# Optimization experiments

Hardware: AMD Instinct MI355X
Metric: run time of the kernel (lower is better)

## Reference

```python
import jax, jax.numpy as jnp
import numpy as np

B, T, SD, AD, H, K, HID = 256, 128, 8, 2, 3, 4, 256


def setup_inputs() -> dict:
    key = jax.random.key(0)
    ks = jax.random.split(key, 12)
    inp = {
        "state": jax.random.normal(ks[0], (B, T, SD), dtype=jnp.float32),
        "action": jax.random.normal(ks[1], (B, T, AD), dtype=jnp.float32),
        # Linear(4, 4*H, bias=False): weight (4*H, 4)
        "Wk": jax.random.normal(ks[2], (4 * H, K), dtype=jnp.float32) * 0.1,
        "Wq": jax.random.normal(ks[3], (4 * H, SD + AD), dtype=jnp.float32) * 0.1,
        "Wv": jax.random.normal(ks[4], (4 * H, K), dtype=jnp.float32) * 0.1,
        # MLP: in_dim = 4*H + SD + AD -> HID -> HID -> 1
        "W1": jax.random.normal(ks[5], (HID, 4 * H + SD + AD), dtype=jnp.float32) * 0.05,
        "b1": jnp.zeros((HID,), dtype=jnp.float32),
        "W2": jax.random.normal(ks[6], (HID, HID), dtype=jnp.float32) * 0.05,
        "b2": jnp.zeros((HID,), dtype=jnp.float32),
        "Wout": jax.random.uniform(ks[7], (1, HID), minval=-0.003, maxval=0.003, dtype=jnp.float32),
        "bout": jax.random.uniform(ks[8], (1,), minval=-0.003, maxval=0.003, dtype=jnp.float32),
    }
    return inp


def reference(state, action, Wk, Wq, Wv, W1, b1, W2, b2, Wout, bout):
    q_state = jnp.concatenate([state, action], axis=-1)  # (b, t, sd+ad)
    s = state[:, :, :4]                                   # (b, t, 4)
    b, t, k = s.shape
    h = Wk.shape[0] // k
    # rel_full[b, i, j] = s[b, j] - s[b, i]  (matches torch view/transpose)
    rel_full = s[:, None, :, :] - s[:, :, None, :]        # (b, t, t, 4)
    # drop diagonal (self-pairs): idx[i] = all j != i, in order
    j = jnp.arange(t - 1)
    idx = j[None, :] + (j[None, :] >= jnp.arange(t)[:, None])  # (t, t-1)
    rel = jnp.take_along_axis(rel_full, idx[None, :, :, None], axis=2)  # (b, t, t-1, 4)
    # QKV projections (tiny head dim k=4)
    q = (q_state @ Wq.T).reshape(b, t, h, k)              # (b, t, h, 4)
    keys = (rel @ Wk.T).reshape(b, t, t - 1, h, k)        # (b, t, t-1, h, 4)
    vals = (rel @ Wv.T).reshape(b, t, t - 1, h, k)
    scores = jnp.einsum('bthk,btjhk->bthj', q, keys) / jnp.sqrt(jnp.float32(k))
    w = jax.nn.softmax(scores, axis=-1)                   # over the t-1 neighbors
    x = jnp.einsum('bthj,btjhk->bthk', w, vals).reshape(b, t, h * k)
    x = jnp.concatenate([x, q_state], axis=-1)            # (b, t, h*4 + sd+ad)
    x = jax.nn.relu(x @ W1.T + b1)
    x = jax.nn.relu(x @ W2.T + b2)
    return x @ Wout.T + bout                              # (b, t, 1)
```

## Files before the change

kernel.cpp:

```cpp
#include <hip/hip_runtime.h>
#include <math.h>

#define Bp 256
#define Tp 128
#define SDp 8
#define ADp 2
#define Hp 3
#define Kp 4
#define HIDp 256
#define QDp (SDp + ADp)
#define X1Dp (Hp * Kp + QDp)
#define QKLD 17
#define LOG2E 1.4426950408889634f

typedef short bf16x8 __attribute__((ext_vector_type(8)));
typedef float f32x4  __attribute__((ext_vector_type(4)));

__device__ __forceinline__ unsigned short f2bf(float f) {
    unsigned u = __float_as_uint(f);
    unsigned r = (u + 0x7FFFu + ((u >> 16) & 1u)) >> 16;
    return (unsigned short)r;
}

__device__ __forceinline__ unsigned h1_byte(int row, int colbytes) {
    return (((unsigned)row << 9) + (unsigned)colbytes) ^ ((unsigned)(row & 7) << 4);
}
__device__ __forceinline__ unsigned x1_byte(int row, int colbytes) {
    return ((unsigned)row << 6) + ((unsigned)colbytes ^ (((unsigned)row & 6u) << 3));
}

__global__ __launch_bounds__(256) void prep_kernel(
    const float* __restrict__ W1, const float* __restrict__ W2,
    unsigned short* __restrict__ W1b, unsigned short* __restrict__ W2b)
{
    const int bid = blockIdx.x;
    const int tid = threadIdx.x;
    if (bid < 64) {
        const int i = bid * 1024 + tid * 4;
        const float4 v = *(const float4*)(W2 + i);
        ushort4 o;
        o.x = f2bf(v.x); o.y = f2bf(v.y); o.z = f2bf(v.z); o.w = f2bf(v.w);
        *(ushort4*)(W2b + i) = o;
    } else {
        const int i = (bid - 64) * 256 + tid;
        const int r = i >> 5, c = i & 31;
        W1b[i] = (c < X1Dp) ? f2bf(W1[r * X1Dp + c]) : (unsigned short)0;
    }
}

__global__ __launch_bounds__(256, 4) void main_kernel(
    const float* __restrict__ state, const float* __restrict__ action,
    const float* __restrict__ Wk, const float* __restrict__ Wq,
    const float* __restrict__ Wv,
    const unsigned short* __restrict__ W1b, const unsigned short* __restrict__ W2b,
    const float* __restrict__ b1, const float* __restrict__ b2,
    const float* __restrict__ Wout, const float* __restrict__ bout,
    float* __restrict__ out)
{
    const int bid   = blockIdx.x;
    const int batch = bid >> 2;
    const int t0    = (bid & 3) * 32;
    const int tid   = threadIdx.x;
    const int lane  = tid & 63;
    const int wave  = tid >> 6;
    const int quad  = lane >> 4;
    const int l16   = lane & 15;
    const int t_loc = tid >> 3;
    const int jo    = tid & 7;
    const int t     = t0 + t_loc;

    __shared__ float4 s4[Tp];
    __shared__ float  wv[Hp * Kp * Kp];
    __shared__ float  qk[32 * QKLD];
    __shared__ float  b1s[HIDp];
    __shared__ float  b2s[HIDp];
    __shared__ float  wouts[HIDp];
    __shared__ __align__(16) unsigned short X1s[32 * 32];
    __shared__ __align__(16) unsigned short h1s[32 * 256];
    __shared__ float partial[4][32];

    const int rt_b  = wave & 1;
    const int chh_b = wave >> 1;
    bf16x8 bfr[8];
    #pragma unroll
    for (int n = 0; n < 8; ++n)
        bfr[n] = *(const bf16x8*)&W1b[(chh_b * 128 + n * 16 + l16) * 32 + quad * 8];
    bf16x8 Bc[4];
    {
        const unsigned short* wr0 = W2b + (size_t)((wave * 4 + 0) * 16 + l16) * HIDp + quad * 8;
        #pragma unroll
        for (int k = 0; k < 4; ++k)
            Bc[k] = *(const bf16x8*)(wr0 + k * 32);
    }

    if (tid < Tp) {
        s4[tid] = ((const float4*)(state + (size_t)batch * Tp * SDp))[tid * 2];
    } else if (tid < 160) {
        const int ta = tid - 128;
        const int tt = t0 + ta;
        float qs[QDp];
        {
            const float* srow = state + ((size_t)batch * Tp + tt) * SDp;
            const float4 v0 = *(const float4*)srow;
            const float4 v1 = *(const float4*)(srow + 4);
            qs[0]=v0.x; qs[1]=v0.y; qs[2]=v0.z; qs[3]=v0.w;
            qs[4]=v1.x; qs[5]=v1.y; qs[6]=v1.z; qs[7]=v1.w;
            const float* arow = action + ((size_t)batch * Tp + tt) * ADp;
            qs[8] = arow[0]; qs[9] = arow[1];
        }
        float q[Hp * Kp];
        #pragma unroll
        for (int r = 0; r < Hp * Kp; ++r) {
            float a = 0.f;
            #pragma unroll
            for (int d = 0; d < QDp; ++d) a += qs[d] * Wq[r * QDp + d];
            q[r] = a;
        }
        float* qrow = &qk[ta * QKLD];
        #pragma unroll
        for (int h = 0; h < Hp; ++h)
            #pragma unroll
            for (int c = 0; c < Kp; ++c) {
                float a = 0.f;
                #pragma unroll
                for (int k = 0; k < Kp; ++k) a += q[h * Kp + k] * Wk[(h * Kp + k) * Kp + c];
                qrow[h * 4 + c] = 0.5f * LOG2E * a;
            }
        #pragma unroll
        for (int i = 0; i < 5; ++i) {
            const unsigned u = (unsigned)f2bf(qs[2*i]) | ((unsigned)f2bf(qs[2*i+1]) << 16);
            qrow[12 + i] = __uint_as_float(u);
        }
    } else if (tid < 160 + Hp * Kp * Kp) {
        wv[tid - 160] = Wv[tid - 160];
    }
    b1s[tid]   = b1[tid];
    b2s[tid]   = b2[tid];
    wouts[tid] = Wout[tid];
    __syncthreads();

    float rq[12];
    #pragma unroll
    for (int i = 0; i < 3; ++i)
        *(float4*)&rq[i * 4] = *(const float4*)&qk[t_loc * QKLD + i * 4];

    float l[Hp] = {0.f, 0.f, 0.f};
    float ac[Hp][4] = {};
    #pragma unroll
    for (int i = 0; i < 16; ++i) {
        const int j = (jo << 4) | ((i + jo) & 15);
        const float4 sj = s4[j];
        #pragma unroll
        for (int h = 0; h < Hp; ++h) {
            const float d = sj.x * rq[h*4] + sj.y * rq[h*4+1]
                          + sj.z * rq[h*4+2] + sj.w * rq[h*4+3];
            const float e = __builtin_amdgcn_exp2f(d);
            l[h] += e;
            ac[h][0] += e * sj.x; ac[h][1] += e * sj.y;
            ac[h][2] += e * sj.z; ac[h][3] += e * sj.w;
        }
    }
    #pragma unroll
    for (int off = 1; off < 8; off <<= 1) {
        #pragma unroll
        for (int h = 0; h < Hp; ++h) {
            l[h] += __shfl_xor(l[h], off);
            #pragma unroll
            for (int c = 0; c < Kp; ++c) ac[h][c] += __shfl_xor(ac[h][c], off);
        }
    }

    if (jo == 0) {
        const float4 st = s4[t];
        unsigned short rowb[32] __attribute__((aligned(16)));
        #pragma unroll
        for (int h = 0; h < Hp; ++h) {
            const float dtt = st.x * rq[h*4] + st.y * rq[h*4+1]
                            + st.z * rq[h*4+2] + st.w * rq[h*4+3];
            const float ett = __builtin_amdgcn_exp2f(dtt);
            const float inv = 1.f / (l[h] - ett);
            const float rb0 = (ac[h][0] - ett * st.x) * inv - st.x;
            const float rb1 = (ac[h][1] - ett * st.y) * inv - st.y;
            const float rb2 = (ac[h][2] - ett * st.z) * inv - st.z;
            const float rb3 = (ac[h][3] - ett * st.w) * inv - st.w;
            #pragma unroll
            for (int k = 0; k < Kp; ++k) {
                const int r = h * Kp + k;
                rowb[r] = f2bf(rb0 * wv[r*4] + rb1 * wv[r*4+1] + rb2 * wv[r*4+2] + rb3 * wv[r*4+3]);
            }
        }
        #pragma unroll
        for (int i = 0; i < 5; ++i) {
            const unsigned u = __float_as_uint(qk[t_loc * QKLD + 12 + i]);
            rowb[12 + 2*i] = (unsigned short)(u & 0xffffu);
            rowb[13 + 2*i] = (unsigned short)(u >> 16);
        }
        #pragma unroll
        for (int i = X1Dp; i < 32; ++i) rowb[i] = 0;

        const uint4* srcv = (const uint4*)rowb;
        #pragma unroll
        for (int i = 0; i < 4; ++i)
            *(uint4*)((char*)X1s + x1_byte(t_loc, i * 16)) = srcv[i];
    }
    __syncthreads();

    {
        const bf16x8 afr = *(const bf16x8*)((const char*)X1s +
                             x1_byte(rt_b * 16 + l16, quad * 16));
        #pragma unroll
        for (int n = 0; n < 8; ++n) {
            const int col = chh_b * 128 + n * 16 + l16;
            f32x4 acc = {0.f, 0.f, 0.f, 0.f};
            acc = __builtin_amdgcn_mfma_f32_16x16x32_bf16(afr, bfr[n], acc, 0, 0, 0);
            const float bb = b1s[col];
            #pragma unroll
            for (int r = 0; r < 4; ++r) {
                const int row = rt_b * 16 + quad * 4 + r;
                *(unsigned short*)((char*)h1s + h1_byte(row, col * 2)) =
                    f2bf(fmaxf(acc[r] + bb, 0.f));
            }
        }
    }
    __syncthreads();

    float rsum[2][4] = {};
    f32x4 acc0 = {0.f, 0.f, 0.f, 0.f};
    f32x4 acc1 = {0.f, 0.f, 0.f, 0.f};
    bf16x8 Bn[4];
    #pragma unroll
    for (int g = 0; g < 8; ++g) {
        const int i  = g >> 1;
        const int hf = g & 1;
        if (g < 7) {
            const int ni  = (g + 1) >> 1;
            const int nhf = (g + 1) & 1;
            const unsigned short* wr = W2b + (size_t)((wave * 4 + ni) * 16 + l16) * HIDp
                                     + nhf * 128 + quad * 8;
            #pragma unroll
            for (int k = 0; k < 4; ++k)
                Bn[k] = *(const bf16x8*)(wr + k * 32);
        }
        #pragma unroll
        for (int k = 0; k < 4; ++k) {
            const int ksg = hf * 4 + k;
            const bf16x8 a0 = *(const bf16x8*)((const char*)h1s +
                                h1_byte(l16,      ksg * 64 + quad * 16));
            const bf16x8 a1 = *(const bf16x8*)((const char*)h1s +
                                h1_byte(16 + l16, ksg * 64 + quad * 16));
            acc0 = __builtin_amdgcn_mfma_f32_16x16x32_bf16(a0, Bc[k], acc0, 0, 0, 0);
            acc1 = __builtin_amdgcn_mfma_f32_16x16x32_bf16(a1, Bc[k], acc1, 0, 0, 0);
        }
        if (hf == 1) {
            const int col = (wave * 4 + i) * 16 + l16;
            const float bb = b2s[col];
            const float wo = wouts[col];
            #pragma unroll
            for (int r = 0; r < 4; ++r) {
                rsum[0][r] += fmaxf(acc0[r] + bb, 0.f) * wo;
                rsum[1][r] += fmaxf(acc1[r] + bb, 0.f) * wo;
            }
            acc0 = (f32x4){0.f, 0.f, 0.f, 0.f};
            acc1 = (f32x4){0.f, 0.f, 0.f, 0.f};
        }
        #pragma unroll
        for (int k = 0; k < 4; ++k) Bc[k] = Bn[k];
    }

    #pragma unroll
    for (int off = 1; off < 16; off <<= 1)
        #pragma unroll
        for (int rt = 0; rt < 2; ++rt)
            #pragma unroll
            for (int r = 0; r < 4; ++r)
                rsum[rt][r] += __shfl_xor(rsum[rt][r], off);

    if (l16 == 0) {
        #pragma unroll
        for (int rt = 0; rt < 2; ++rt)
            #pragma unroll
            for (int r = 0; r < 4; ++r)
                partial[wave][rt * 16 + quad * 4 + r] = rsum[rt][r];
    }
    __syncthreads();

    if (tid < 32) {
        out[(size_t)batch * Tp + t0 + tid] =
            partial[0][tid] + partial[1][tid] + partial[2][tid]
          + partial[3][tid] + bout[0];
    }
}

extern "C" void kernel_launch(void* const* d_in, const int* in_sizes, int n_in,
                              void* d_out, int out_size, void* d_ws, size_t ws_size,
                              hipStream_t stream) {
    const float* state  = (const float*)d_in[0];
    const float* action = (const float*)d_in[1];
    const float* Wk     = (const float*)d_in[2];
    const float* Wq     = (const float*)d_in[3];
    const float* Wv     = (const float*)d_in[4];
    const float* W1     = (const float*)d_in[5];
    const float* b1     = (const float*)d_in[6];
    const float* W2     = (const float*)d_in[7];
    const float* b2     = (const float*)d_in[8];
    const float* Wout   = (const float*)d_in[9];
    const float* bout   = (const float*)d_in[10];
    float* out = (float*)d_out;

    char* ws = (char*)d_ws;
    unsigned short* W1b = (unsigned short*)(ws);
    unsigned short* W2b = (unsigned short*)(ws + 16384);

    prep_kernel<<<96, 256, 0, stream>>>(W1, W2, W1b, W2b);
    main_kernel<<<4 * Bp, 256, 0, stream>>>(state, action, Wk, Wq, Wv,
                                            W1b, W2b, b1, b2, Wout, bout, out);
}
```

Baseline: 109.0 us.

## Fuse weight bf16 conversion into main kernel and drop prep kernel

Removes the separate prep kernel that converted W1 and W2 to bf16. Each block now converts W1 into a swizzled shared-memory tile and converts fp32 W2 fragments in registers with v_cvt_pk_bf16_f32 just before each MFMA. Bias and Wout are read straight from global memory instead of being staged in shared memory. This saves one kernel launch and the workspace round trip, but every block reads twice as many fp32 W2 bytes, repeats the conversion work, and uses more LDS and registers.

```diff
diff --git a/kernel.cpp b/kernel.cpp
--- a/kernel.cpp
+++ b/kernel.cpp
@@ -22,40 +22,26 @@
     return (unsigned short)r;
 }
 
+__device__ __forceinline__ unsigned cvtpk(float lo, float hi) {
+    unsigned r;
+    asm("v_cvt_pk_bf16_f32 %0, %1, %2" : "=v"(r) : "v"(lo), "v"(hi));
+    return r;
+}
+
 __device__ __forceinline__ unsigned h1_byte(int row, int colbytes) {
     return (((unsigned)row << 9) + (unsigned)colbytes) ^ ((unsigned)(row & 7) << 4);
 }
 __device__ __forceinline__ unsigned x1_byte(int row, int colbytes) {
     return ((unsigned)row << 6) + ((unsigned)colbytes ^ (((unsigned)row & 6u) << 3));
-}
-
-__global__ __launch_bounds__(256) void prep_kernel(
-    const float* __restrict__ W1, const float* __restrict__ W2,
-    unsigned short* __restrict__ W1b, unsigned short* __restrict__ W2b)
-{
-    const int bid = blockIdx.x;
-    const int tid = threadIdx.x;
-    if (bid < 64) {
-        const int i = bid * 1024 + tid * 4;
-        const float4 v = *(const float4*)(W2 + i);
-        ushort4 o;
-        o.x = f2bf(v.x); o.y = f2bf(v.y); o.z = f2bf(v.z); o.w = f2bf(v.w);
-        *(ushort4*)(W2b + i) = o;
-    } else {
-        const int i = (bid - 64) * 256 + tid;
-        const int r = i >> 5, c = i & 31;
-        W1b[i] = (c < X1Dp) ? f2bf(W1[r * X1Dp + c]) : (unsigned short)0;
-    }
 }
 
 __global__ __launch_bounds__(256, 4) void main_kernel(
     const float* __restrict__ state, const float* __restrict__ action,
     const float* __restrict__ Wk, const float* __restrict__ Wq,
-    const float* __restrict__ Wv,
-    const unsigned short* __restrict__ W1b, const unsigned short* __restrict__ W2b,
-    const float* __restrict__ b1, const float* __restrict__ b2,
-    const float* __restrict__ Wout, const float* __restrict__ bout,
-    float* __restrict__ out)
+    const float* __restrict__ Wv, const float* __restrict__ W1,
+    const float* __restrict__ b1, const float* __restrict__ W2,
+    const float* __restrict__ b2, const float* __restrict__ Wout,
+    const float* __restrict__ bout, float* __restrict__ out)
 {
     const int bid   = blockIdx.x;
     const int batch = bid >> 2;
@@ -72,26 +58,10 @@
     __shared__ float4 s4[Tp];
     __shared__ float  wv[Hp * Kp * Kp];
     __shared__ float  qk[32 * QKLD];
-    __shared__ float  b1s[HIDp];
-    __shared__ float  b2s[HIDp];
-    __shared__ float  wouts[HIDp];
     __shared__ __align__(16) unsigned short X1s[32 * 32];
+    __shared__ __align__(16) unsigned short W1s[256 * 32];
     __shared__ __align__(16) unsigned short h1s[32 * 256];
     __shared__ float partial[4][32];
-
-    const int rt_b  = wave & 1;
-    const int chh_b = wave >> 1;
-    bf16x8 bfr[8];
-    #pragma unroll
-    for (int n = 0; n < 8; ++n)
-        bfr[n] = *(const bf16x8*)&W1b[(chh_b * 128 + n * 16 + l16) * 32 + quad * 8];
-    bf16x8 Bc[4];
-    {
-        const unsigned short* wr0 = W2b + (size_t)((wave * 4 + 0) * 16 + l16) * HIDp + quad * 8;
-        #pragma unroll
-        for (int k = 0; k < 4; ++k)
-            Bc[k] = *(const bf16x8*)(wr0 + k * 32);
-    }
 
     if (tid < Tp) {
         s4[tid] = ((const float4*)(state + (size_t)batch * Tp * SDp))[tid * 2];
@@ -127,16 +97,29 @@
                 qrow[h * 4 + c] = 0.5f * LOG2E * a;
             }
         #pragma unroll
-        for (int i = 0; i < 5; ++i) {
-            const unsigned u = (unsigned)f2bf(qs[2*i]) | ((unsigned)f2bf(qs[2*i+1]) << 16);
-            qrow[12 + i] = __uint_as_float(u);
-        }
+        for (int i = 0; i < 5; ++i)
+            qrow[12 + i] = __uint_as_float(cvtpk(qs[2*i], qs[2*i+1]));
     } else if (tid < 160 + Hp * Kp * Kp) {
         wv[tid - 160] = Wv[tid - 160];
     }
-    b1s[tid]   = b1[tid];
-    b2s[tid]   = b2[tid];
-    wouts[tid] = Wout[tid];
+    {
+        const float* wr = W1 + tid * X1Dp;
+        float w[22];
+        #pragma unroll
+        for (int i = 0; i < 11; ++i) {
+            const float2 v = *(const float2*)(wr + i * 2);
+            w[2*i] = v.x; w[2*i+1] = v.y;
+        }
+        unsigned rb[16];
+        #pragma unroll
+        for (int i = 0; i < 11; ++i) rb[i] = cvtpk(w[2*i], w[2*i+1]);
+        #pragma unroll
+        for (int i = 11; i < 16; ++i) rb[i] = 0u;
+        const uint4* sv = (const uint4*)rb;
+        #pragma unroll
+        for (int i = 0; i < 4; ++i)
+            *(uint4*)((char*)W1s + x1_byte(tid, i * 16)) = sv[i];
+    }
     __syncthreads();
 
     float rq[12];
@@ -206,17 +189,24 @@
     __syncthreads();
 
     {
+        const int rt  = wave & 1;
+        const int chh = wave >> 1;
+        bf16x8 bfr[8];
+        #pragma unroll
+        for (int n = 0; n < 8; ++n)
+            bfr[n] = *(const bf16x8*)((const char*)W1s +
+                       x1_byte(chh * 128 + n * 16 + l16, quad * 16));
         const bf16x8 afr = *(const bf16x8*)((const char*)X1s +
-                             x1_byte(rt_b * 16 + l16, quad * 16));
+                             x1_byte(rt * 16 + l16, quad * 16));
         #pragma unroll
         for (int n = 0; n < 8; ++n) {
-            const int col = chh_b * 128 + n * 16 + l16;
+            const int col = chh * 128 + n * 16 + l16;
             f32x4 acc = {0.f, 0.f, 0.f, 0.f};
             acc = __builtin_amdgcn_mfma_f32_16x16x32_bf16(afr, bfr[n], acc, 0, 0, 0);
-            const float bb = b1s[col];
+            const float bb = b1[col];
             #pragma unroll
             for (int r = 0; r < 4; ++r) {
-                const int row = rt_b * 16 + quad * 4 + r;
+                const int row = rt * 16 + quad * 4 + r;
                 *(unsigned short*)((char*)h1s + h1_byte(row, col * 2)) =
                     f2bf(fmaxf(acc[r] + bb, 0.f));
             }
@@ -227,34 +217,50 @@
     float rsum[2][4] = {};
     f32x4 acc0 = {0.f, 0.f, 0.f, 0.f};
     f32x4 acc1 = {0.f, 0.f, 0.f, 0.f};
-    bf16x8 Bn[4];
-    #pragma unroll
-    for (int g = 0; g < 8; ++g) {
-        const int i  = g >> 1;
-        const int hf = g & 1;
-        if (g < 7) {
-            const int ni  = (g + 1) >> 1;
-            const int nhf = (g + 1) & 1;
-            const unsigned short* wr = W2b + (size_t)((wave * 4 + ni) * 16 + l16) * HIDp
-                                     + nhf * 128 + quad * 8;
-            #pragma unroll
-            for (int k = 0; k < 4; ++k)
-                Bn[k] = *(const bf16x8*)(wr + k * 32);
-        }
-        #pragma unroll
-        for (int k = 0; k < 4; ++k) {
-            const int ksg = hf * 4 + k;
+    float4 sg[8];
+    {
+        const float* wp = W2 + (size_t)(wave * 64 + l16) * HIDp + quad * 8;
+        #pragma unroll
+        for (int m = 0; m < 4; ++m) {
+            sg[2*m]   = *(const float4*)(wp + m * 32);
+            sg[2*m+1] = *(const float4*)(wp + m * 32 + 4);
+        }
+    }
+    #pragma unroll
+    for (int k = 0; k < 8; ++k) {
+        const int i  = k >> 1;
+        const int hf = k & 1;
+        float4 nx[8];
+        if (k < 7) {
+            const int ni  = (k + 1) >> 1;
+            const int nhf = (k + 1) & 1;
+            const float* wp = W2 + (size_t)((wave * 4 + ni) * 16 + l16) * HIDp
+                            + nhf * 128 + quad * 8;
+            #pragma unroll
+            for (int m = 0; m < 4; ++m) {
+                nx[2*m]   = *(const float4*)(wp + m * 32);
+                nx[2*m+1] = *(const float4*)(wp + m * 32 + 4);
+            }
+        }
+        #pragma unroll
+        for (int m = 0; m < 4; ++m) {
+            union { unsigned u[4]; bf16x8 v; } cv;
+            cv.u[0] = cvtpk(sg[2*m].x,   sg[2*m].y);
+            cv.u[1] = cvtpk(sg[2*m].z,   sg[2*m].w);
+            cv.u[2] = cvtpk(sg[2*m+1].x, sg[2*m+1].y);
+            cv.u[3] = cvtpk(sg[2*m+1].z, sg[2*m+1].w);
+            const int ks = hf * 4 + m;
             const bf16x8 a0 = *(const bf16x8*)((const char*)h1s +
-                                h1_byte(l16,      ksg * 64 + quad * 16));
+                                h1_byte(l16,      ks * 64 + quad * 16));
             const bf16x8 a1 = *(const bf16x8*)((const char*)h1s +
-                                h1_byte(16 + l16, ksg * 64 + quad * 16));
-            acc0 = __builtin_amdgcn_mfma_f32_16x16x32_bf16(a0, Bc[k], acc0, 0, 0, 0);
-            acc1 = __builtin_amdgcn_mfma_f32_16x16x32_bf16(a1, Bc[k], acc1, 0, 0, 0);
+                                h1_byte(16 + l16, ks * 64 + quad * 16));
+            acc0 = __builtin_amdgcn_mfma_f32_16x16x32_bf16(a0, cv.v, acc0, 0, 0, 0);
+            acc1 = __builtin_amdgcn_mfma_f32_16x16x32_bf16(a1, cv.v, acc1, 0, 0, 0);
         }
         if (hf == 1) {
             const int col = (wave * 4 + i) * 16 + l16;
-            const float bb = b2s[col];
-            const float wo = wouts[col];
+            const float bb = b2[col];
+            const float wo = Wout[col];
             #pragma unroll
             for (int r = 0; r < 4; ++r) {
                 rsum[0][r] += fmaxf(acc0[r] + bb, 0.f) * wo;
@@ -264,7 +270,7 @@
             acc1 = (f32x4){0.f, 0.f, 0.f, 0.f};
         }
         #pragma unroll
-        for (int k = 0; k < 4; ++k) Bc[k] = Bn[k];
+        for (int m = 0; m < 8; ++m) sg[m] = nx[m];
     }
 
     #pragma unroll
@@ -307,11 +313,8 @@
     const float* bout   = (const float*)d_in[10];
     float* out = (float*)d_out;
 
-    char* ws = (char*)d_ws;
-    unsigned short* W1b = (unsigned short*)(ws);
-    unsigned short* W2b = (unsigned short*)(ws + 16384);
-
-    prep_kernel<<<96, 256, 0, stream>>>(W1, W2, W1b, W2b);
+    (void)d_ws; (void)ws_size;
+
     main_kernel<<<4 * Bp, 256, 0, stream>>>(state, action, Wk, Wq, Wv,
-                                            W1b, W2b, b1, b2, Wout, bout, out);
-}
+                                            W1, b1, W2, b2, Wout, bout, out);
+}
```

New measurement: 108.5 us. Within noise of the previous version (-0.4%).
